# Kernel tuning notes

Hardware: AMD Instinct MI355X
Metric: run time of the kernel (lower is better)

## Reference

```python
import jax, jax.numpy as jnp
import numpy as np

I, H = 4, 64


def setup_inputs() -> dict:
    key = jax.random.key(0)
    ks = jax.random.split(key, 7)
    s_ih = 1.0 / np.sqrt(H)
    return {
        "x": jax.random.normal(ks[0], (8192, 512, I), dtype=jnp.float32),
        "W_ih": jax.random.uniform(ks[1], (4 * H, I), minval=-s_ih, maxval=s_ih, dtype=jnp.float32),
        "W_hh": jax.random.uniform(ks[2], (4 * H, H), minval=-s_ih, maxval=s_ih, dtype=jnp.float32),
        "b_ih": jax.random.uniform(ks[3], (4 * H,), minval=-s_ih, maxval=s_ih, dtype=jnp.float32),
        "b_hh": jax.random.uniform(ks[4], (4 * H,), minval=-s_ih, maxval=s_ih, dtype=jnp.float32),
        "W_fc": jax.random.uniform(ks[5], (1, H), minval=-s_ih, maxval=s_ih, dtype=jnp.float32),
        "b_fc": jax.random.uniform(ks[6], (1,), minval=-s_ih, maxval=s_ih, dtype=jnp.float32),
    }


def _lstm_last_hidden(x, W_ih, W_hh, b_ih, b_hh):
    # x: [B, T, I] batch_first; PyTorch gate order: i, f, g, o
    B = x.shape[0]
    # Precompute input projections for all timesteps in one GEMM: [T, B, 4H]
    xg = jnp.einsum('bti,gi->tbg', x, W_ih) + (b_ih + b_hh)

    def step(carry, xg_t):
        h, c = carry
        gates = xg_t + h @ W_hh.T  # [B, 4H]
        i, f, g, o = jnp.split(gates, 4, axis=-1)
        i = jax.nn.sigmoid(i)
        f = jax.nn.sigmoid(f)
        g = jnp.tanh(g)
        o = jax.nn.sigmoid(o)
        c = f * c + i * g
        h = o * jnp.tanh(c)
        return (h, c), None

    h0 = jnp.zeros((B, W_hh.shape[1]), dtype=x.dtype)
    c0 = jnp.zeros_like(h0)
    (h_n, _), _ = jax.lax.scan(step, (h0, c0), xg)
    return h_n  # [B, H]


def reference(x, W_ih, W_hh, b_ih, b_hh, W_fc, b_fc):
    h_n = _lstm_last_hidden(x, W_ih, W_hh, b_ih, b_hh)
    return h_n @ W_fc.T + b_fc  # [B, 1]
```

## Files before the change

### kernel.cpp

```cpp
#include <hip/hip_runtime.h>


typedef float f32x4 __attribute__((ext_vector_type(4)));
typedef float f32x2 __attribute__((ext_vector_type(2)));
typedef _Float16 f16x8 __attribute__((ext_vector_type(8)));
typedef _Float16 f16x4 __attribute__((ext_vector_type(4)));

#define TSEQ 512
#define IDIM 4
#define BPB 16
#define TCH 32
#define NCH (TSEQ / TCH)
#define L2E 1.44269504088896340736f

#if __has_builtin(__builtin_amdgcn_exp2f)
#define EX2(v) __builtin_amdgcn_exp2f(v)
#else
#define EX2(v) exp2f(v)
#endif
#define RCP(v) __builtin_amdgcn_rcpf(v)

#define STEP_BARRIER() do {                                   \
    asm volatile("s_waitcnt lgkmcnt(0)" ::: "memory");        \
    __builtin_amdgcn_s_barrier();                             \
} while (0)

__global__ __launch_bounds__(256, 2) void lstm_fused(
    const float* __restrict__ x,
    const float* __restrict__ W_ih,
    const float* __restrict__ W_hh,
    const float* __restrict__ b_ih,
    const float* __restrict__ b_hh,
    const float* __restrict__ W_fc,
    const float* __restrict__ b_fc,
    float* __restrict__ out)
{
    __shared__ __align__(16) _Float16 hbuf[2][BPB * 64];
    __shared__ __align__(16) f16x4    xstage[2][BPB][33];

    const int tid  = threadIdx.x;
    const int lane = tid & 63;
    const int wv   = tid >> 6;
    const int b0   = blockIdx.x * BPB;
    const int r    = lane & 15;
    const int g16  = lane >> 4;

    f16x8 bfrag[4][3];
    #pragma unroll
    for (int t4 = 0; t4 < 4; ++t4) {
        const float sc = (t4 == 2) ? 2.0f * L2E : L2E;
        const int g = t4 * 64 + wv * 16 + r;
        #pragma unroll
        for (int ks = 0; ks < 2; ++ks) {
            const float* p = W_hh + g * 64 + ks * 32 + g16 * 8;
            f16x8 f;
            #pragma unroll
            for (int j = 0; j < 8; ++j) f[j] = (_Float16)(p[j] * sc);
            bfrag[t4][ks] = f;
        }
        f16x8 f;
        #pragma unroll
        for (int j = 0; j < 8; ++j) f[j] = (_Float16)0.0f;
        if (g16 == 0) {
            #pragma unroll
            for (int j = 0; j < 4; ++j) f[j] = (_Float16)(W_ih[g * IDIM + j] * sc);
            float biasf = (b_ih[g] + b_hh[g]) * sc;
            _Float16 hi = (_Float16)biasf;
            f[4] = hi;
            f[5] = (_Float16)(biasf - (float)hi);
        }
        bfrag[t4][2] = f;
    }
    const float wfc = W_fc[lane];
    const float bfc = b_fc[0];
    const f32x4 zero4 = {0.f, 0.f, 0.f, 0.f};

    float c_reg[4] = {0.f, 0.f, 0.f, 0.f};
    for (int i = tid; i < BPB * 64; i += 256) hbuf[0][i] = (_Float16)0.0f;

    const int bb0 = tid >> 5, tf = tid & 31;
    const float* xg0 = x + ((size_t)(b0 + bb0)     * TSEQ + tf) * IDIM;
    const float* xg1 = x + ((size_t)(b0 + bb0 + 8) * TSEQ + tf) * IDIM;
    float4 xn0 = *(const float4*)xg0;
    float4 xn1 = *(const float4*)xg1;
    {
        f16x4 s0, s1;
        s0[0] = (_Float16)xn0.x; s0[1] = (_Float16)xn0.y;
        s0[2] = (_Float16)xn0.z; s0[3] = (_Float16)xn0.w;
        s1[0] = (_Float16)xn1.x; s1[1] = (_Float16)xn1.y;
        s1[2] = (_Float16)xn1.z; s1[3] = (_Float16)xn1.w;
        xstage[0][bb0][tf]     = s0;
        xstage[0][bb0 + 8][tf] = s1;
    }
    __syncthreads();
    xn0 = *(const float4*)(xg0 + TCH * IDIM);
    xn1 = *(const float4*)(xg1 + TCH * IDIM);

    if (((blockIdx.x ^ (blockIdx.x >> 8)) & 1) != 0)
        __builtin_amdgcn_s_sleep(13);

    const int hbase = r * 128;
    const int hs0 = ((g16 + 0) << 4) ^ ((r & 7) << 4);
    const int hs1 = ((g16 + 4) << 4) ^ ((r & 7) << 4);
    int hw[4];
    #pragma unroll
    for (int q = 0; q < 4; ++q) {
        const int bat = 4 * g16 + q;
        hw[q] = (bat * 128 + (wv * 16 + r) * 2) ^ ((bat & 7) << 4);
    }
    char* hbB = (char*)&hbuf[0][0];
    const char* xsB = (const char*)&xstage[0][0][0];
    const int xrow = r * 33 * 8;

    f16x4 xv = *(const f16x4*)(xsB + xrow);

    auto cellpair = [&](const f32x4* acc, int q0, int q1, char* wb) {
        f32x2 ei, ef, eg, eo;
        ei[0] = EX2(-acc[0][q0]); ei[1] = EX2(-acc[0][q1]);
        ef[0] = EX2(-acc[1][q0]); ef[1] = EX2(-acc[1][q1]);
        eg[0] = EX2(-acc[2][q0]); eg[1] = EX2(-acc[2][q1]);
        eo[0] = EX2(-acc[3][q0]); eo[1] = EX2(-acc[3][q1]);
        const f32x2 one = {1.f, 1.f};
        f32x2 A  = one + ei, F = one + ef;
        f32x2 Gp = one + eg, Gm = one - eg;
        f32x2 P2 = A * Gp;
        f32x2 cr = { c_reg[q0], c_reg[q1] };
        f32x2 num = cr * P2 + Gm * F;
        f32x2 den = P2 * F;
        f32x2 rd; rd[0] = RCP(den[0]); rd[1] = RCP(den[1]);
        f32x2 c = num * rd;
        c_reg[q0] = c[0]; c_reg[q1] = c[1];
        f32x2 uc = c * (2.0f * L2E);
        uc = __builtin_elementwise_max(uc, f32x2{-60.f, -60.f});
        f32x2 et; et[0] = EX2(-uc[0]); et[1] = EX2(-uc[1]);
        f32x2 hd = (one + eo) * (one + et);
        f32x2 rh; rh[0] = RCP(hd[0]); rh[1] = RCP(hd[1]);
        f32x2 h = (one - et) * rh;
        *(_Float16*)(wb + hw[q0]) = (_Float16)h[0];
        *(_Float16*)(wb + hw[q1]) = (_Float16)h[1];
    };

    auto substep = [&](int t, int P) {
        const char* rb = hbB + P * 2048;
        char*       wb = hbB + (P ^ 1) * 2048;
        f16x8 a0 = *(const f16x8*)(rb + hbase + hs0);
        f16x8 a1 = *(const f16x8*)(rb + hbase + hs1);
        f16x8 ax;
        ax[0] = xv[0]; ax[1] = xv[1]; ax[2] = xv[2]; ax[3] = xv[3];
        ax[4] = (_Float16)1.0f; ax[5] = (_Float16)1.0f;
        ax[6] = (_Float16)0.0f; ax[7] = (_Float16)0.0f;

        f32x4 acc[4];
        __builtin_amdgcn_s_setprio(1);
        #pragma unroll
        for (int t4 = 0; t4 < 4; ++t4) {
            f32x4 a;
            a = __builtin_amdgcn_mfma_f32_16x16x32_f16(a0, bfrag[t4][0], zero4, 0, 0, 0);
            a = __builtin_amdgcn_mfma_f32_16x16x32_f16(a1, bfrag[t4][1], a, 0, 0, 0);
            a = __builtin_amdgcn_mfma_f32_16x16x32_f16(ax, bfrag[t4][2], a, 0, 0, 0);
            acc[t4] = a;
        }
        __builtin_amdgcn_s_setprio(0);

        const int tn = t + 1;
        xv = *(const f16x4*)(xsB + ((tn >> 5) & 1) * 4224 + xrow + (tn & 31) * 8);

        cellpair(acc, 0, 1, wb);
        cellpair(acc, 2, 3, wb);
        STEP_BARRIER();
    };

    for (int t = 0; t < TSEQ; t += 2) {
        if ((t & (TCH - 1)) == 16) {
            const int c = t >> 5;
            if (c + 1 < NCH) {
                f16x4 s0, s1;
                s0[0] = (_Float16)xn0.x; s0[1] = (_Float16)xn0.y;
                s0[2] = (_Float16)xn0.z; s0[3] = (_Float16)xn0.w;
                s1[0] = (_Float16)xn1.x; s1[1] = (_Float16)xn1.y;
                s1[2] = (_Float16)xn1.z; s1[3] = (_Float16)xn1.w;
                f16x4* dst = &xstage[(c + 1) & 1][0][0];
                dst[bb0 * 33 + tf]       = s0;
                dst[(bb0 + 8) * 33 + tf] = s1;
                if (c + 2 < NCH) {
                    xn0 = *(const float4*)(xg0 + (size_t)(c + 2) * TCH * IDIM);
                    xn1 = *(const float4*)(xg1 + (size_t)(c + 2) * TCH * IDIM);
                }
            }
        }
        substep(t,     0);
        substep(t + 1, 1);
    }

    #pragma unroll
    for (int q = 0; q < 4; ++q) {
        const int bat  = wv * 4 + q;
        const int byte = (bat * 128 + lane * 2) ^ ((bat & 7) << 4);
        float hv = (float)*(const _Float16*)(hbB + byte);
        float partial = hv * wfc;
        #pragma unroll
        for (int off = 32; off > 0; off >>= 1)
            partial += __shfl_down(partial, off);
        if (lane == 0) out[b0 + bat] = partial + bfc;
    }
}

extern "C" void kernel_launch(void* const* d_in, const int* in_sizes, int n_in,
                              void* d_out, int out_size, void* d_ws, size_t ws_size,
                              hipStream_t stream) {
    const float* x    = (const float*)d_in[0];
    const float* W_ih = (const float*)d_in[1];
    const float* W_hh = (const float*)d_in[2];
    const float* b_ih = (const float*)d_in[3];
    const float* b_hh = (const float*)d_in[4];
    const float* W_fc = (const float*)d_in[5];
    const float* b_fc = (const float*)d_in[6];
    float* out = (float*)d_out;

    const int B = in_sizes[0] / (TSEQ * IDIM);
    lstm_fused<<<B / BPB, 256, 0, stream>>>(x, W_ih, W_hh, b_ih, b_hh, W_fc, b_fc, out);
}
```

Before: 311.5 us.

## Merge two 16-batch groups into one 512-thread block sharing barriers

Each block now processes 32 batch rows as two independent 256-thread groups with separate h and x staging buffers, launched as 512-thread blocks with one block per CU in launch bounds. The per-step barrier now covers both groups, so one group's MFMA work can overlap the other's transcendental work within a block, replacing the staggered-sleep trick between co-resident blocks. It also halves the block count. The cost is that the barrier spans eight waves instead of four, so a slow wave stalls more work.

Result: no change. 317.2 us (+1.8%).

```diff
diff --git a/kernel.cpp b/kernel.cpp
--- a/kernel.cpp
+++ b/kernel.cpp
@@ -8,7 +8,7 @@
 
 #define TSEQ 512
 #define IDIM 4
-#define BPB 16
+#define BPB 32
 #define TCH 32
 #define NCH (TSEQ / TCH)
 #define L2E 1.44269504088896340736f
@@ -25,7 +25,7 @@
     __builtin_amdgcn_s_barrier();                             \
 } while (0)
 
-__global__ __launch_bounds__(256, 2) void lstm_fused(
+__global__ __launch_bounds__(512, 1) void lstm_fused(
     const float* __restrict__ x,
     const float* __restrict__ W_ih,
     const float* __restrict__ W_hh,
@@ -35,12 +35,13 @@
     const float* __restrict__ b_fc,
     float* __restrict__ out)
 {
-    __shared__ __align__(16) _Float16 hbuf[2][BPB * 64];
-    __shared__ __align__(16) f16x4    xstage[2][BPB][33];
+    __shared__ __align__(16) _Float16 hbuf[2][2][16 * 64];
+    __shared__ __align__(16) f16x4    xstage[2][2][16][33];
 
     const int tid  = threadIdx.x;
     const int lane = tid & 63;
-    const int wv   = tid >> 6;
+    const int wvl  = (tid >> 6) & 3;
+    const int grp  = tid >> 8;
     const int b0   = blockIdx.x * BPB;
     const int r    = lane & 15;
     const int g16  = lane >> 4;
@@ -49,7 +50,7 @@
     #pragma unroll
     for (int t4 = 0; t4 < 4; ++t4) {
         const float sc = (t4 == 2) ? 2.0f * L2E : L2E;
-        const int g = t4 * 64 + wv * 16 + r;
+        const int g = t4 * 64 + wvl * 16 + r;
         #pragma unroll
         for (int ks = 0; ks < 2; ++ks) {
             const float* p = W_hh + g * 64 + ks * 32 + g16 * 8;
@@ -76,11 +77,12 @@
     const f32x4 zero4 = {0.f, 0.f, 0.f, 0.f};
 
     float c_reg[4] = {0.f, 0.f, 0.f, 0.f};
-    for (int i = tid; i < BPB * 64; i += 256) hbuf[0][i] = (_Float16)0.0f;
+    for (int i = tid; i < 2 * 16 * 64; i += 512)
+        ((_Float16*)&hbuf[0][0][0])[i] = (_Float16)0.0f;
 
     const int bb0 = tid >> 5, tf = tid & 31;
-    const float* xg0 = x + ((size_t)(b0 + bb0)     * TSEQ + tf) * IDIM;
-    const float* xg1 = x + ((size_t)(b0 + bb0 + 8) * TSEQ + tf) * IDIM;
+    const float* xg0 = x + ((size_t)(b0 + bb0)      * TSEQ + tf) * IDIM;
+    const float* xg1 = x + ((size_t)(b0 + 16 + bb0) * TSEQ + tf) * IDIM;
     float4 xn0 = *(const float4*)xg0;
     float4 xn1 = *(const float4*)xg1;
     {
@@ -89,15 +91,12 @@
         s0[2] = (_Float16)xn0.z; s0[3] = (_Float16)xn0.w;
         s1[0] = (_Float16)xn1.x; s1[1] = (_Float16)xn1.y;
         s1[2] = (_Float16)xn1.z; s1[3] = (_Float16)xn1.w;
-        xstage[0][bb0][tf]     = s0;
-        xstage[0][bb0 + 8][tf] = s1;
+        xstage[0][0][bb0][tf] = s0;
+        xstage[1][0][bb0][tf] = s1;
     }
     __syncthreads();
     xn0 = *(const float4*)(xg0 + TCH * IDIM);
     xn1 = *(const float4*)(xg1 + TCH * IDIM);
-
-    if (((blockIdx.x ^ (blockIdx.x >> 8)) & 1) != 0)
-        __builtin_amdgcn_s_sleep(13);
 
     const int hbase = r * 128;
     const int hs0 = ((g16 + 0) << 4) ^ ((r & 7) << 4);
@@ -106,10 +105,10 @@
     #pragma unroll
     for (int q = 0; q < 4; ++q) {
         const int bat = 4 * g16 + q;
-        hw[q] = (bat * 128 + (wv * 16 + r) * 2) ^ ((bat & 7) << 4);
-    }
-    char* hbB = (char*)&hbuf[0][0];
-    const char* xsB = (const char*)&xstage[0][0][0];
+        hw[q] = (bat * 128 + (wvl * 16 + r) * 2) ^ ((bat & 7) << 4);
+    }
+    char* hbG = (char*)&hbuf[0][0][0] + grp * 2048;
+    const char* xsB = (const char*)&xstage[grp][0][0][0];
     const int xrow = r * 33 * 8;
 
     f16x4 xv = *(const f16x4*)(xsB + xrow);
@@ -141,8 +140,8 @@
     };
 
     auto substep = [&](int t, int P) {
-        const char* rb = hbB + P * 2048;
-        char*       wb = hbB + (P ^ 1) * 2048;
+        const char* rb = hbG + P * 4096;
+        char*       wb = hbG + (P ^ 1) * 4096;
         f16x8 a0 = *(const f16x8*)(rb + hbase + hs0);
         f16x8 a1 = *(const f16x8*)(rb + hbase + hs1);
         f16x8 ax;
@@ -179,9 +178,9 @@
                 s0[2] = (_Float16)xn0.z; s0[3] = (_Float16)xn0.w;
                 s1[0] = (_Float16)xn1.x; s1[1] = (_Float16)xn1.y;
                 s1[2] = (_Float16)xn1.z; s1[3] = (_Float16)xn1.w;
-                f16x4* dst = &xstage[(c + 1) & 1][0][0];
-                dst[bb0 * 33 + tf]       = s0;
-                dst[(bb0 + 8) * 33 + tf] = s1;
+                const int nb = (c + 1) & 1;
+                xstage[0][nb][bb0][tf] = s0;
+                xstage[1][nb][bb0][tf] = s1;
                 if (c + 2 < NCH) {
                     xn0 = *(const float4*)(xg0 + (size_t)(c + 2) * TCH * IDIM);
                     xn1 = *(const float4*)(xg1 + (size_t)(c + 2) * TCH * IDIM);
@@ -194,14 +193,14 @@
 
     #pragma unroll
     for (int q = 0; q < 4; ++q) {
-        const int bat  = wv * 4 + q;
+        const int bat  = wvl * 4 + q;
         const int byte = (bat * 128 + lane * 2) ^ ((bat & 7) << 4);
-        float hv = (float)*(const _Float16*)(hbB + byte);
+        float hv = (float)*(const _Float16*)(hbG + byte);
         float partial = hv * wfc;
         #pragma unroll
         for (int off = 32; off > 0; off >>= 1)
             partial += __shfl_down(partial, off);
-        if (lane == 0) out[b0 + bat] = partial + bfc;
+        if (lane == 0) out[b0 + grp * 16 + bat] = partial + bfc;
     }
 }
 
@@ -218,5 +217,5 @@
     float* out = (float*)d_out;
 
     const int B = in_sizes[0] / (TSEQ * IDIM);
-    lstm_fused<<<B / BPB, 256, 0, stream>>>(x, W_ih, W_hh, b_ih, b_hh, W_fc, b_fc, out);
+    lstm_fused<<<B / BPB, 512, 0, stream>>>(x, W_ih, W_hh, b_ih, b_hh, W_fc, b_fc, out);
 }
```
